# Kernel optimization log

Hardware: AMD Instinct MI355X
Metric: run time of the kernel (lower is better)

Reference implementation:

```python
import jax, jax.numpy as jnp
import numpy as np

SHRINKAGE = 0.1  # matches init_kwargs shrinkage_rate


def setup_inputs() -> dict:
    key = jax.random.key(0)
    k0, k1, k2, k3 = jax.random.split(key, 4)
    B, F, T, D, P = 8192, 256, 32, 6, 8
    N = 2 ** D - 1  # internal nodes per tree
    L = 2 ** D      # leaves per tree
    return {
        "x": jax.random.normal(k0, (B, F), dtype=jnp.float32),
        "W": jax.random.normal(k1, (T, N, F), dtype=jnp.float32) / np.float32(np.sqrt(F)),
        "b": jax.random.normal(k2, (T, N), dtype=jnp.float32) * 0.01,
        "phi": jax.random.normal(k3, (T, L, P), dtype=jnp.float32),
    }


def reference(x, W, b, phi):
    # x: [B,F]; W: [T,N,F]; b: [T,N]; phi: [T,L,P]
    T, N, F = W.shape
    L = N + 1
    D = int(round(np.log2(L)))
    # all node gating probabilities in one batched GEMM: p(right) per internal node
    s = jax.nn.sigmoid(jnp.einsum('bf,tnf->btn', x, W) + b)  # [B,T,N]
    # heap (level-order) node indexing: node at level d with prefix q has index 2^d-1+q;
    # leaf l's bit at level d is (l >> (D-1-d)) & 1 (1 -> right child -> prob s, 0 -> 1-s)
    leaves = np.arange(L)
    leaf_prob = jnp.ones(s.shape[:2] + (L,), dtype=s.dtype)  # [B,T,L]
    for d in range(D):  # static small loop over tree depth
        bits = jnp.asarray((leaves >> (D - 1 - d)) & 1, dtype=bool)
        idx = (2 ** d - 1) + (leaves >> (D - d))
        sd = s[:, :, idx]  # [B,T,L]
        leaf_prob = leaf_prob * jnp.where(bits, sd, 1.0 - sd)
    # per-tree prediction = sum_l path_prob_l * phi_l; GBM output = shrinkage * sum_t
    tree_pred = jnp.einsum('btl,tlp->btp', leaf_prob, phi)  # [B,T,P]
    return SHRINKAGE * tree_pred.sum(axis=1)  # [B,P]
```

## Files before the change

### kernel.cpp

```cpp
#include <hip/hip_runtime.h>

#define B_TOT   8192
#define F_DIM   256
#define T_TREES 32
#define N_NODES 63
#define P_DIM   8
#define BM      128
#define SHRINK  0.1f

typedef __bf16 bf16_t;
typedef bf16_t bf16x8 __attribute__((ext_vector_type(8)));
typedef float  f32x4  __attribute__((ext_vector_type(4)));
typedef unsigned short ushort8_t __attribute__((ext_vector_type(8)));
typedef unsigned short ushort4_t __attribute__((ext_vector_type(4)));

__device__ __forceinline__ unsigned short f2bf(float f) {
    unsigned int u = __float_as_uint(f);
    u += 0x7fffu + ((u >> 16) & 1u);
    return (unsigned short)(u >> 16);
}
__device__ __forceinline__ unsigned int pk2bf(float a, float b) {
    unsigned int ua = __float_as_uint(a); ua += 0x7fffu + ((ua >> 16) & 1u);
    unsigned int ub = __float_as_uint(b); ub += 0x7fffu + ((ub >> 16) & 1u);
    return (ua >> 16) | (ub & 0xffff0000u);
}
__device__ __forceinline__ void gl_lds16(const void* g, void* l) {
    __builtin_amdgcn_global_load_lds(
        (const __attribute__((address_space(1))) unsigned int*)g,
        (__attribute__((address_space(3))) unsigned int*)l, 16, 0, 0);
}

__global__ __launch_bounds__(256) void cvt_all(
    const float* __restrict__ x, const float* __restrict__ W,
    const float* __restrict__ phi,
    unsigned short* __restrict__ xb, unsigned short* __restrict__ Wb,
    unsigned short* __restrict__ phiB)
{
    const int bx  = blockIdx.x;
    const int tid = threadIdx.x;
    if (bx < 2048) {
        const int i = bx * 256 + tid;
        const float4 v = *(const float4*)&x[(size_t)i * 4];
        ushort4_t h;
        h.x = f2bf(v.x); h.y = f2bf(v.y); h.z = f2bf(v.z); h.w = f2bf(v.w);
        *(ushort4_t*)&xb[(size_t)i * 4] = h;
    } else if (bx < 2560) {
        const int i = (bx - 2048) * 256 + tid;
        const int tree = i >> 12;
        const int rem  = i & 4095;
        const int row  = rem >> 6;
        const int c4   = rem & 63;
        float4 v = make_float4(0.f, 0.f, 0.f, 0.f);
        if (row < N_NODES)
            v = *(const float4*)&W[((size_t)(tree * N_NODES + row)) * F_DIM + c4 * 4];
        ushort4_t h;
        h.x = f2bf(v.x); h.y = f2bf(v.y); h.z = f2bf(v.z); h.w = f2bf(v.w);
        *(ushort4_t*)&Wb[(size_t)i * 4] = h;
    } else {
        const int i = (bx - 2560) * 256 + tid;
        const int tree = i >> 7;
        const int rem  = i & 127;
        const int k2   = rem >> 6;
        const int lane = rem & 63;
        const int lm   = lane & 15;
        const int quad = lane >> 4;
        ushort8_t h;
#pragma unroll
        for (int j = 0; j < 8; ++j) {
            float v = 0.f;
            if (lm < 8) v = phi[(size_t)tree * 512 + (k2 * 32 + quad * 8 + j) * 8 + lm];
            h[j] = f2bf(v);
        }
        *(ushort8_t*)&phiB[(size_t)i * 8] = h;
    }
}

__global__ __launch_bounds__(256, 3) void softgbm_main(
    const unsigned short* __restrict__ xb, const unsigned short* __restrict__ Wb,
    const unsigned short* __restrict__ phiB, const float* __restrict__ bias,
    float* __restrict__ out)
{
    __shared__ union Smem {
        struct { unsigned short A[BM * 64]; unsigned short B[BM * 64]; } g;
        unsigned short ss[2][BM * 64];
    } sm;
    __shared__ unsigned short lv[BM * 64];
    __shared__ float bs2[2][64];

    const int tid  = threadIdx.x;
    const int tp   = blockIdx.x;
    const int b0   = blockIdx.y * BM;
    const int wave = tid >> 6;
    const int lane = tid & 63;
    const int quad = lane >> 4;
    const int lm   = lane & 15;
    const int wr   = wave >> 1;
    const int wc   = wave & 1;

    if (tid < 128) {
        const int p = tid >> 6, node = tid & 63;
        bs2[p][node] = (node < N_NODES) ? bias[(tp * 2 + p) * N_NODES + node] : 0.f;
    }

    f32x4 acc[4][4];
#pragma unroll
    for (int m = 0; m < 4; ++m)
#pragma unroll
        for (int n = 0; n < 4; ++n)
            acc[m][n] = f32x4{0.f, 0.f, 0.f, 0.f};

    for (int ko = 0; ko < F_DIM; ko += 64) {
        __syncthreads();
#pragma unroll
        for (int i = 0; i < 4; ++i) {
            const int r = wave * 32 + i * 8 + (lane >> 3);
            const int c = (lane & 7) ^ (r & 7);
            gl_lds16(&xb[(size_t)(b0 + r) * F_DIM + ko + c * 8],
                     &sm.g.A[(wave * 32 + i * 8) * 64]);
        }
#pragma unroll
        for (int i = 0; i < 4; ++i) {
            const int r = wave * 32 + i * 8 + (lane >> 3);
            const int c = (lane & 7) ^ (r & 7);
            gl_lds16(&Wb[(size_t)(tp * 128 + r) * F_DIM + ko + c * 8],
                     &sm.g.B[(wave * 32 + i * 8) * 64]);
        }
        __syncthreads();

#pragma unroll
        for (int ks = 0; ks < 2; ++ks) {
            bf16x8 af[4], bfr[4];
#pragma unroll
            for (int m = 0; m < 4; ++m) {
                const int r  = wr * 64 + m * 16 + lm;
                const int cp = (ks * 4 + quad) ^ (r & 7);
                af[m] = __builtin_bit_cast(bf16x8, *(ushort8_t*)&sm.g.A[r * 64 + cp * 8]);
            }
#pragma unroll
            for (int n = 0; n < 4; ++n) {
                const int r  = wc * 64 + n * 16 + lm;
                const int cp = (ks * 4 + quad) ^ (r & 7);
                bfr[n] = __builtin_bit_cast(bf16x8, *(ushort8_t*)&sm.g.B[r * 64 + cp * 8]);
            }
#pragma unroll
            for (int m = 0; m < 4; ++m)
#pragma unroll
                for (int n = 0; n < 4; ++n)
                    acc[m][n] = __builtin_amdgcn_mfma_f32_16x16x32_bf16(af[m], bfr[n], acc[m][n], 0, 0, 0);
        }
    }
    __syncthreads();

    bf16x8 pb[2][2];
#pragma unroll
    for (int p = 0; p < 2; ++p)
#pragma unroll
        for (int k2 = 0; k2 < 2; ++k2)
            pb[p][k2] = __builtin_bit_cast(bf16x8,
                *(const ushort8_t*)&phiB[(size_t)(((tp * 2 + p) * 2 + k2) * 64 + lane) * 8]);

#pragma unroll
    for (int m = 0; m < 4; ++m)
#pragma unroll
        for (int n = 0; n < 4; ++n) {
            const int node = n * 16 + lm;
            const float bb = bs2[wc][node];
#pragma unroll
            for (int reg = 0; reg < 4; ++reg) {
                const int row = wr * 64 + m * 16 + quad * 4 + reg;
                const float z = acc[m][n][reg] + bb;
                const float s = __frcp_rn(1.0f + __expf(-z));
                const int slot = (node >> 3) ^ (row & 7);
                sm.ss[wc][row * 64 + slot * 8 + (node & 7)] = f2bf(s);
            }
        }
    __syncthreads();

    f32x4 accp[2] = { f32x4{0.f,0.f,0.f,0.f}, f32x4{0.f,0.f,0.f,0.f} };

    const int row = tid >> 1;
    const int h   = tid & 1;
    const int rs  = row & 7;

    for (int p = 0; p < 2; ++p) {
        const unsigned short* sp = &sm.ss[p][row * 64];
        unsigned int cw[32];
#pragma unroll
        for (int c = 0; c < 8; ++c)
            *(uint4*)&cw[c * 4] = *(const uint4*)&sp[(c ^ rs) * 8];

#define NV(j) ((j) & 1 ? __uint_as_float(cw[(j) >> 1] & 0xffff0000u) \
                       : __uint_as_float(cw[(j) >> 1] << 16))
#define SEL(a, b) (h ? NV(b) : NV(a))
        const float s0v = NV(0);
        const float q1  = h ? s0v : (1.0f - s0v);
        float q2[2], q3[4], q4[8], q5[16], q6[32];
        {
            const float t = SEL(1, 2);
            q2[1] = q1 * t; q2[0] = q1 - q2[1];
        }
#pragma unroll
        for (int v = 0; v < 2; ++v) {
            const float t = SEL(3 + v, 5 + v);
            q3[2 * v + 1] = q2[v] * t; q3[2 * v] = q2[v] - q3[2 * v + 1];
        }
#pragma unroll
        for (int v = 0; v < 4; ++v) {
            const float t = SEL(7 + v, 11 + v);
            q4[2 * v + 1] = q3[v] * t; q4[2 * v] = q3[v] - q4[2 * v + 1];
        }
#pragma unroll
        for (int v = 0; v < 8; ++v) {
            const float t = SEL(15 + v, 23 + v);
            q5[2 * v + 1] = q4[v] * t; q5[2 * v] = q4[v] - q5[2 * v + 1];
        }
#pragma unroll
        for (int v = 0; v < 16; ++v) {
            const float t = SEL(31 + v, 47 + v);
            q6[2 * v + 1] = q5[v] * t; q6[2 * v] = q5[v] - q6[2 * v + 1];
        }
#undef SEL
#undef NV
#pragma unroll
        for (int i = 0; i < 4; ++i) {
            uint4 w;
            w.x = pk2bf(q6[i * 8 + 0], q6[i * 8 + 1]);
            w.y = pk2bf(q6[i * 8 + 2], q6[i * 8 + 3]);
            w.z = pk2bf(q6[i * 8 + 4], q6[i * 8 + 5]);
            w.w = pk2bf(q6[i * 8 + 6], q6[i * 8 + 7]);
            *(uint4*)&lv[row * 64 + (((h * 4 + i) ^ rs)) * 8] = w;
        }
        __syncthreads();

#pragma unroll
        for (int mg = 0; mg < 2; ++mg) {
#pragma unroll
            for (int k2 = 0; k2 < 2; ++k2) {
                const int r2 = wave * 32 + mg * 16 + lm;
                const int cp = (k2 * 4 + quad) ^ (r2 & 7);
                const bf16x8 afr = __builtin_bit_cast(bf16x8,
                    *(ushort8_t*)&lv[r2 * 64 + cp * 8]);
                accp[mg] = __builtin_amdgcn_mfma_f32_16x16x32_bf16(afr, pb[p][k2], accp[mg], 0, 0, 0);
            }
        }
        __syncthreads();
    }

    if (lm < P_DIM) {
#pragma unroll
        for (int mg = 0; mg < 2; ++mg)
#pragma unroll
            for (int reg = 0; reg < 4; ++reg) {
                const int r2 = wave * 32 + mg * 16 + quad * 4 + reg;
                atomicAdd(&out[(size_t)(b0 + r2) * P_DIM + lm], SHRINK * accp[mg][reg]);
            }
    }
}

extern "C" void kernel_launch(void* const* d_in, const int* in_sizes, int n_in,
                              void* d_out, int out_size, void* d_ws, size_t ws_size,
                              hipStream_t stream) {
    const float* x    = (const float*)d_in[0];
    const float* W    = (const float*)d_in[1];
    const float* bias = (const float*)d_in[2];
    const float* phi  = (const float*)d_in[3];
    float* out = (float*)d_out;

    unsigned short* xb   = (unsigned short*)d_ws;
    unsigned short* Wb   = xb + (size_t)B_TOT * F_DIM;
    unsigned short* phiB = Wb + (size_t)T_TREES * 64 * F_DIM;

    hipMemsetAsync(out, 0, sizeof(float) * B_TOT * P_DIM, stream);
    cvt_all<<<dim3(2576), dim3(256), 0, stream>>>(x, W, phi, xb, Wb, phiB);

    dim3 grid(T_TREES / 2, B_TOT / BM);
    softgbm_main<<<grid, dim3(256), 0, stream>>>(xb, Wb, phiB, bias, out);
}
```

Measured before the change: 91.45 us.

## Split fused GEMM-sigmoid and tree-walk kernel into two kernels via workspace

The single fused kernel becomes two. The first does the GEMM plus sigmoid and writes bf16 gate probabilities to a global workspace, reordered so each half-tree walker reads contiguous values. The second kernel, launched one block per tree per batch tile, expands leaf probabilities and runs the phi MFMA with atomic accumulation. The aim is to raise occupancy (launch bounds go from 3 to 4) and drop the LDS and registers the tree walk needed inside the GEMM kernel. The cost is an extra global round trip of about 33 MB, one more kernel launch, and twice as many atomics.

Result: slower. 107.2 us (+17.2%).

```diff
diff --git a/kernel.cpp b/kernel.cpp
--- a/kernel.cpp
+++ b/kernel.cpp
@@ -6,6 +6,7 @@
 #define N_NODES 63
 #define P_DIM   8
 #define BM      128
+#define SCAT_LD 72
 #define SHRINK  0.1f
 
 typedef __bf16 bf16_t;
@@ -75,16 +76,14 @@
     }
 }
 
-__global__ __launch_bounds__(256, 3) void softgbm_main(
+__global__ __launch_bounds__(256, 4) void gemm_sig(
     const unsigned short* __restrict__ xb, const unsigned short* __restrict__ Wb,
-    const unsigned short* __restrict__ phiB, const float* __restrict__ bias,
-    float* __restrict__ out)
+    const float* __restrict__ bias, unsigned short* __restrict__ s_ws)
 {
     __shared__ union Smem {
         struct { unsigned short A[BM * 64]; unsigned short B[BM * 64]; } g;
-        unsigned short ss[2][BM * 64];
+        unsigned short scat[2 * BM * SCAT_LD];
     } sm;
-    __shared__ unsigned short lv[BM * 64];
     __shared__ float bs2[2][64];
 
     const int tid  = threadIdx.x;
@@ -151,13 +150,21 @@
     }
     __syncthreads();
 
-    bf16x8 pb[2][2];
-#pragma unroll
-    for (int p = 0; p < 2; ++p)
-#pragma unroll
-        for (int k2 = 0; k2 < 2; ++k2)
-            pb[p][k2] = __builtin_bit_cast(bf16x8,
-                *(const ushort8_t*)&phiB[(size_t)(((tp * 2 + p) * 2 + k2) * 64 + lane) * 8]);
+    int slot[4];
+#pragma unroll
+    for (int n = 0; n < 4; ++n) {
+        const int node = n * 16 + lm;
+        const int np1  = node + 1;
+        const int d    = 31 - __builtin_clz(np1);
+        if (d == 0) slot[n] = 0;
+        else {
+            const int half = 1 << (d - 1);
+            const int u    = np1 - (1 << d);
+            const int hh   = (u >= half) ? 1 : 0;
+            const int pos  = half + (u & (half - 1));
+            slot[n] = hh * 32 + pos;
+        }
+    }
 
 #pragma unroll
     for (int m = 0; m < 4; ++m)
@@ -169,82 +176,113 @@
             for (int reg = 0; reg < 4; ++reg) {
                 const int row = wr * 64 + m * 16 + quad * 4 + reg;
                 const float z = acc[m][n][reg] + bb;
-                const float s = __frcp_rn(1.0f + __expf(-z));
-                const int slot = (node >> 3) ^ (row & 7);
-                sm.ss[wc][row * 64 + slot * 8 + (node & 7)] = f2bf(s);
+                const unsigned short sv = f2bf(__frcp_rn(1.0f + __expf(-z)));
+                if (node < N_NODES) {
+                    unsigned short* base = &sm.scat[(wc * BM + row) * SCAT_LD];
+                    base[slot[n]] = sv;
+                    if (node == 0) base[32] = sv;
+                }
             }
         }
     __syncthreads();
 
-    f32x4 accp[2] = { f32x4{0.f,0.f,0.f,0.f}, f32x4{0.f,0.f,0.f,0.f} };
+#pragma unroll
+    for (int i = 0; i < 8; ++i) {
+        const int c  = i * 256 + tid;
+        const int p  = c >> 10;
+        const int rr = (c >> 3) & 127;
+        const int g  = c & 7;
+        const uint4 v = *(const uint4*)&sm.scat[(p * BM + rr) * SCAT_LD + g * 8];
+        *(uint4*)&s_ws[((size_t)(tp * 2 + p) * B_TOT + b0 + rr) * 64 + g * 8] = v;
+    }
+}
+
+__global__ __launch_bounds__(256, 4) void walk_phi(
+    const unsigned short* __restrict__ s_ws, const unsigned short* __restrict__ phiB,
+    float* __restrict__ out)
+{
+    __shared__ unsigned short lv[BM * 64];
+
+    const int tid  = threadIdx.x;
+    const int t    = blockIdx.x;
+    const int b0   = blockIdx.y * BM;
+    const int wave = tid >> 6;
+    const int lane = tid & 63;
+    const int quad = lane >> 4;
+    const int lm   = lane & 15;
 
     const int row = tid >> 1;
     const int h   = tid & 1;
     const int rs  = row & 7;
 
-    for (int p = 0; p < 2; ++p) {
-        const unsigned short* sp = &sm.ss[p][row * 64];
-        unsigned int cw[32];
-#pragma unroll
-        for (int c = 0; c < 8; ++c)
-            *(uint4*)&cw[c * 4] = *(const uint4*)&sp[(c ^ rs) * 8];
-
-#define NV(j) ((j) & 1 ? __uint_as_float(cw[(j) >> 1] & 0xffff0000u) \
-                       : __uint_as_float(cw[(j) >> 1] << 16))
-#define SEL(a, b) (h ? NV(b) : NV(a))
-        const float s0v = NV(0);
-        const float q1  = h ? s0v : (1.0f - s0v);
-        float q2[2], q3[4], q4[8], q5[16], q6[32];
-        {
-            const float t = SEL(1, 2);
-            q2[1] = q1 * t; q2[0] = q1 - q2[1];
-        }
-#pragma unroll
-        for (int v = 0; v < 2; ++v) {
-            const float t = SEL(3 + v, 5 + v);
-            q3[2 * v + 1] = q2[v] * t; q3[2 * v] = q2[v] - q3[2 * v + 1];
-        }
-#pragma unroll
-        for (int v = 0; v < 4; ++v) {
-            const float t = SEL(7 + v, 11 + v);
-            q4[2 * v + 1] = q3[v] * t; q4[2 * v] = q3[v] - q4[2 * v + 1];
-        }
-#pragma unroll
-        for (int v = 0; v < 8; ++v) {
-            const float t = SEL(15 + v, 23 + v);
-            q5[2 * v + 1] = q4[v] * t; q5[2 * v] = q4[v] - q5[2 * v + 1];
-        }
-#pragma unroll
-        for (int v = 0; v < 16; ++v) {
-            const float t = SEL(31 + v, 47 + v);
-            q6[2 * v + 1] = q5[v] * t; q6[2 * v] = q5[v] - q6[2 * v + 1];
-        }
-#undef SEL
-#undef NV
-#pragma unroll
-        for (int i = 0; i < 4; ++i) {
-            uint4 w;
-            w.x = pk2bf(q6[i * 8 + 0], q6[i * 8 + 1]);
-            w.y = pk2bf(q6[i * 8 + 2], q6[i * 8 + 3]);
-            w.z = pk2bf(q6[i * 8 + 4], q6[i * 8 + 5]);
-            w.w = pk2bf(q6[i * 8 + 6], q6[i * 8 + 7]);
-            *(uint4*)&lv[row * 64 + (((h * 4 + i) ^ rs)) * 8] = w;
-        }
-        __syncthreads();
-
-#pragma unroll
-        for (int mg = 0; mg < 2; ++mg) {
-#pragma unroll
-            for (int k2 = 0; k2 < 2; ++k2) {
-                const int r2 = wave * 32 + mg * 16 + lm;
-                const int cp = (k2 * 4 + quad) ^ (r2 & 7);
-                const bf16x8 afr = __builtin_bit_cast(bf16x8,
-                    *(ushort8_t*)&lv[r2 * 64 + cp * 8]);
-                accp[mg] = __builtin_amdgcn_mfma_f32_16x16x32_bf16(afr, pb[p][k2], accp[mg], 0, 0, 0);
-            }
-        }
-        __syncthreads();
-    }
+    unsigned int w[16];
+    {
+        const unsigned short* sp = &s_ws[((size_t)t * B_TOT + b0 + row) * 64 + h * 32];
+        *(uint4*)&w[0]  = *(const uint4*)&sp[0];
+        *(uint4*)&w[4]  = *(const uint4*)&sp[8];
+        *(uint4*)&w[8]  = *(const uint4*)&sp[16];
+        *(uint4*)&w[12] = *(const uint4*)&sp[24];
+    }
+#define VAL(j) ((j) & 1 ? __uint_as_float(w[(j) >> 1] & 0xffff0000u) \
+                        : __uint_as_float(w[(j) >> 1] << 16))
+    const float s0 = VAL(0);
+    const float q1 = h ? s0 : (1.0f - s0);
+    float q2[2], q3[4], q4[8], q5[16], q6[32];
+    {
+        const float tv = VAL(1);
+        q2[1] = q1 * tv; q2[0] = q1 - q2[1];
+    }
+#pragma unroll
+    for (int v = 0; v < 2; ++v) {
+        const float tv = VAL(2 + v);
+        q3[2 * v + 1] = q2[v] * tv; q3[2 * v] = q2[v] - q3[2 * v + 1];
+    }
+#pragma unroll
+    for (int v = 0; v < 4; ++v) {
+        const float tv = VAL(4 + v);
+        q4[2 * v + 1] = q3[v] * tv; q4[2 * v] = q3[v] - q4[2 * v + 1];
+    }
+#pragma unroll
+    for (int v = 0; v < 8; ++v) {
+        const float tv = VAL(8 + v);
+        q5[2 * v + 1] = q4[v] * tv; q5[2 * v] = q4[v] - q5[2 * v + 1];
+    }
+#pragma unroll
+    for (int v = 0; v < 16; ++v) {
+        const float tv = VAL(16 + v);
+        q6[2 * v + 1] = q5[v] * tv; q6[2 * v] = q5[v] - q6[2 * v + 1];
+    }
+#undef VAL
+
+#pragma unroll
+    for (int i = 0; i < 4; ++i) {
+        uint4 wv;
+        wv.x = pk2bf(q6[i * 8 + 0], q6[i * 8 + 1]);
+        wv.y = pk2bf(q6[i * 8 + 2], q6[i * 8 + 3]);
+        wv.z = pk2bf(q6[i * 8 + 4], q6[i * 8 + 5]);
+        wv.w = pk2bf(q6[i * 8 + 6], q6[i * 8 + 7]);
+        *(uint4*)&lv[row * 64 + ((h * 4 + i) ^ rs) * 8] = wv;
+    }
+
+    bf16x8 pb[2];
+#pragma unroll
+    for (int k2 = 0; k2 < 2; ++k2)
+        pb[k2] = __builtin_bit_cast(bf16x8,
+            *(const ushort8_t*)&phiB[(size_t)((t * 2 + k2) * 64 + lane) * 8]);
+
+    __syncthreads();
+
+    f32x4 accp[2] = { f32x4{0.f,0.f,0.f,0.f}, f32x4{0.f,0.f,0.f,0.f} };
+#pragma unroll
+    for (int mg = 0; mg < 2; ++mg)
+#pragma unroll
+        for (int k2 = 0; k2 < 2; ++k2) {
+            const int r2 = wave * 32 + mg * 16 + lm;
+            const int cp = (k2 * 4 + quad) ^ (r2 & 7);
+            const bf16x8 afr = __builtin_bit_cast(bf16x8,
+                *(ushort8_t*)&lv[r2 * 64 + cp * 8]);
+            accp[mg] = __builtin_amdgcn_mfma_f32_16x16x32_bf16(afr, pb[k2], accp[mg], 0, 0, 0);
+        }
 
     if (lm < P_DIM) {
 #pragma unroll
@@ -269,10 +307,11 @@
     unsigned short* xb   = (unsigned short*)d_ws;
     unsigned short* Wb   = xb + (size_t)B_TOT * F_DIM;
     unsigned short* phiB = Wb + (size_t)T_TREES * 64 * F_DIM;
+    unsigned short* s_ws = phiB + (size_t)T_TREES * 2 * 64 * 8;
 
     hipMemsetAsync(out, 0, sizeof(float) * B_TOT * P_DIM, stream);
     cvt_all<<<dim3(2576), dim3(256), 0, stream>>>(x, W, phi, xb, Wb, phiB);
 
-    dim3 grid(T_TREES / 2, B_TOT / BM);
-    softgbm_main<<<grid, dim3(256), 0, stream>>>(xb, Wb, phiB, bias, out);
-}
+    gemm_sig<<<dim3(T_TREES / 2, B_TOT / BM), dim3(256), 0, stream>>>(xb, Wb, bias, s_ws);
+    walk_phi<<<dim3(T_TREES, B_TOT / BM), dim3(256), 0, stream>>>(s_ws, phiB, out);
+}
```
